# Performance work log

Measured on AMD Instinct MI355X. Metric: run time of the kernel, lower is better.

The kernel has to match this reference:

```python
import jax, jax.numpy as jnp
import numpy as np

N_QUBITS = 12
N_LAYERS = 4
BATCH = 4096
DIM = 2 ** N_QUBITS  # 4096


def _apply_1q(state, U, q):
    """Apply 2x2 complex gate U to qubit q. state: (B,) + (2,)*n, wire 0 = MSB (axis q+1)."""
    state = jnp.moveaxis(state, q + 1, -1)
    state = state @ U.T
    return jnp.moveaxis(state, -1, q + 1)


def _apply_cnot(state, c, t):
    """CNOT with control c, target t: flip target amplitudes where control bit == 1."""
    flipped = jnp.flip(state, axis=t + 1)
    shape = [2 if i == c + 1 else 1 for i in range(state.ndim)]
    ctrl = jnp.arange(2).reshape(shape)
    return jnp.where(ctrl == 1, flipped, state)


def setup_inputs() -> dict:
    key = jax.random.key(0)
    k1, k2 = jax.random.split(key)
    x = jax.random.normal(k1, (BATCH, DIM), dtype=jnp.float32)
    weights = jax.random.normal(k2, (N_LAYERS, N_QUBITS, 2), dtype=jnp.float32) * 0.1
    return {"x": x, "weights": weights}


def reference(x, weights):
    n, L = N_QUBITS, N_LAYERS
    B = x.shape[0]
    # AmplitudeEmbedding with normalize=True
    norm = jnp.linalg.norm(x, axis=-1, keepdims=True)
    state = (x / norm).astype(jnp.complex64).reshape((B,) + (2,) * n)
    for layer in range(L):
        for q in range(n):
            ty = weights[layer, q, 0]
            tz = weights[layer, q, 1]
            c, s = jnp.cos(ty / 2), jnp.sin(ty / 2)
            em = jnp.exp(-0.5j * tz.astype(jnp.complex64))  # e^{-i tz/2}
            ep = jnp.exp(+0.5j * tz.astype(jnp.complex64))
            # U = RZ(tz) @ RY(ty), fused single 2x2 gate per qubit
            U = jnp.stack([
                jnp.stack([c * em, -s * em]),
                jnp.stack([s * ep, c * ep]),
            ]).astype(jnp.complex64)
            state = _apply_1q(state, U, q)
        for q in range(n - 1):
            state = _apply_cnot(state, q, q + 1)
        if n > 2:
            state = _apply_cnot(state, n - 1, 0)
    probs = jnp.abs(state) ** 2  # (B,) + (2,)*n, float32
    reduce_axes = tuple(range(1, probs.ndim))
    outs = []
    for q in range(n):
        shape = [2 if i == q + 1 else 1 for i in range(probs.ndim)]
        sign = jnp.array([1.0, -1.0], dtype=probs.dtype).reshape(shape)
        outs.append(jnp.sum(probs * sign, axis=reduce_axes))
    return jnp.stack(outs, axis=-1)  # (B, n_qubits) <Z_q> expvals
```

## Files before the change

### kernel.cpp

```cpp
#include <hip/hip_runtime.h>

#define NQ   12
#define DIM  4096
#define NL   4
#define BLK  512

typedef unsigned short u16;
typedef unsigned int   u32;
typedef float f2 __attribute__((ext_vector_type(2)));

static constexpr int par(u32 v){ return __builtin_popcount(v)&1; }
static constexpr int hb(u16 v){ for(int i=11;i>=0;--i) if((v>>i)&1u) return i; return -1; }

struct L12 { u16 b[NQ]; };

static constexpr u32 lap(const L12& A, u32 x){ u32 r=0; for(int p=0;p<NQ;++p) if((x>>p)&1u) r^=A.b[p]; return r; }
static constexpr L12 lcomp(const L12& A, const L12& B){ L12 r{}; for(int p=0;p<NQ;++p) r.b[p]=(u16)lap(A,(u32)B.b[p]); return r; }
static constexpr L12 lident(){ L12 r{}; for(int p=0;p<NQ;++p) r.b[p]=(u16)(1u<<p); return r; }

static constexpr u32 applyT(u32 i){
  i ^= ((i>>0)&1u) << 11;
  for(int q=10;q>=0;--q){ int pc2=11-q, pt=10-q; i ^= ((i>>pc2)&1u) << pt; }
  return i;
}
static constexpr L12 lT(){ L12 t{}; for(int p=0;p<NQ;++p) t.b[p]=(u16)applyT(1u<<p); return t; }

static constexpr L12 linv(const L12& A){
  u16 v[NQ]={}; u16 u[NQ]={};
  for(int p=0;p<NQ;++p){ v[p]=A.b[p]; u[p]=(u16)(1u<<p); }
  for(int t=0;t<NQ;++t){
    int p=t; while(!((v[p]>>t)&1u)) ++p;
    u16 tv=v[p]; v[p]=v[t]; v[t]=tv; u16 tu=u[p]; u[p]=u[t]; u[t]=tu;
    for(int k=0;k<NQ;++k) if(k!=t && ((v[k]>>t)&1u)){ v[k]^=v[t]; u[k]^=u[t]; }
  }
  L12 r{}; for(int p=0;p<NQ;++p) r.b[p]=u[p]; return r;
}
static constexpr L12 ltr(const L12& A){
  L12 r{}; for(int p=0;p<NQ;++p) for(int q=0;q<NQ;++q) if((A.b[p]>>q)&1u) r.b[q]=(u16)(r.b[q]|(1u<<p));
  return r;
}

struct Tables {
  u16 cm[12][16];
  u16 wg[12][4];
  u16 wexp[NQ];
};

static constexpr Tables make_tables(){
  Tables tb{};
  const L12 T   = lT();
  const L12 Tit = ltr(linv(T));
  L12 A = lident();
  L12 W = lident();
  for(int l=0;l<NL;++l){
    for(int g=0;g<3;++g){
      const int st = l*3+g;
      u16 mm[4]={0,0,0,0};
      for(int i=0;i<4;++i){ mm[i]=A.b[4*g+i]; tb.wg[st][i]=W.b[4*g+i]; }
      for(int c=0;c<16;++c){ u32 m=0; for(int i=0;i<4;++i) if((c>>i)&1) m^=mm[i]; tb.cm[st][c]=(u16)m; }
    }
    A = lcomp(A, T);
    W = lcomp(W, Tit);
  }
  for(int p=0;p<NQ;++p) tb.wexp[p]=W.b[p];
  return tb;
}

static constexpr u16 UIMG[12] = {1,2,4,8, 3,5,6,7, 9,10,11,13};
static constexpr u32 swz(u32 j){
  u32 f=0;
  for(int k=4;k<12;++k) if((j>>k)&1u) f ^= (u32)UIMG[k];
  return j ^ (f & 15u);
}

struct Ech { u16 s[12]; };
static constexpr u16 ered(const Ech& e, u16 x){
  while(x){
    const int lb=hb(x);
    if(e.s[lb]) x=(u16)(x^e.s[lb]); else break;
  }
  return x;
}
static constexpr bool eadd(Ech& e, u16 x){
  x=ered(e,x); if(!x) return false;
  e.s[hb(x)]=x; return true;
}

struct Trip {
  u32 lane_c[9];
  u32 raw9[9];
  u32 smb[3];
  u32 rawm[3];
  u32 scmb[8];
  u32 cinv[3];
  u32 rho[3];
  bool cok;
};

static constexpr Trip make_trip(int t){
  Trip r{};
  const Tables tb = make_tables();
  u16 M[3]={}, w[3]={};
  for(int j=0;j<3;++j){
    const int g=3*t+j, st=g>>2, qi=g&3;
    M[j]=tb.cm[st][(u32)1<<qi]; w[j]=tb.wg[st][qi];
  }
  Ech em{};
  for(int j=0;j<3;++j) eadd(em,M[j]);
  bool isp[12]={};
  for(int b2=0;b2<12;++b2) if(em.s[b2]) isp[b2]=true;
  int np[12]={}; int nn=0;
  for(int p=0;p<12;++p) if(!isp[p]) np[nn++]=p;
  int s0=0,s1=1,s2=2,s3=3; bool found=false;
  for(int i0=0;i0<nn&&!found;++i0)for(int i1=i0+1;i1<nn&&!found;++i1)
  for(int i2=i1+1;i2<nn&&!found;++i2)for(int i3=i2+1;i3<nn&&!found;++i3){
    u16 img[4]={(u16)(swz((u32)1<<np[i0])&15u),(u16)(swz((u32)1<<np[i1])&15u),
                (u16)(swz((u32)1<<np[i2])&15u),(u16)(swz((u32)1<<np[i3])&15u)};
    u16 bas[4]={0,0,0,0}; int rk=0;
    for(int ii=0;ii<4;++ii){
      u16 x=img[ii];
      while(x){
        int hbx=3; while(hbx>0 && !((x>>hbx)&1)) --hbx;
        if(bas[hbx]) x=(u16)(x^bas[hbx]); else { bas[hbx]=x; ++rk; x=0; }
      }
    }
    if(rk==4){ s0=i0;s1=i1;s2=i2;s3=i3; found=true; }
  }
  int ord[9]={}; ord[0]=s0;ord[1]=s1;ord[2]=s2;ord[3]=s3;
  int rp=4;
  for(int j=0;j<nn;++j){ if(j!=s0&&j!=s1&&j!=s2&&j!=s3) ord[rp++]=j; }
  for(int k=0;k<9;++k){
    const int f=np[ord[k]];
    u32 nib=0;
    for(int i=0;i<3;++i) nib |= (u32)((w[i]>>f)&1u)<<i;
    r.lane_c[k]=(swz((u32)1<<f)<<3)|(nib<<28);
    r.raw9[k]=(u32)1<<f;
  }
  for(int k=0;k<3;++k){ r.smb[k]=swz((u32)M[k])<<3; r.rawm[k]=(u32)M[k]; }
  for(int c=0;c<8;++c){
    u32 m=0;
    for(int j=0;j<3;++j) if((c>>j)&1) m^=(u32)M[j];
    r.scmb[c]=swz(m)<<3;
  }
  u32 beta[3]={};
  for(int i=0;i<3;++i){ u32 row=0; for(int k=0;k<3;++k) row|=(u32)par((u32)(M[k]&w[i]))<<k; beta[i]=row; }
  u32 rows[3]={ beta[0]|(1u<<3), beta[1]|(2u<<3), beta[2]|(4u<<3) };
  bool ok=true;
  for(int col=0;col<3;++col){
    int pv=-1;
    for(int rr=col;rr<3;++rr) if((rows[rr]>>col)&1u){pv=rr;break;}
    if(pv<0){ok=false;break;}
    u32 tt=rows[col]; rows[col]=rows[pv]; rows[pv]=tt;
    for(int rr=0;rr<3;++rr) if(rr!=col&&((rows[rr]>>col)&1u)) rows[rr]^=rows[col];
  }
  r.cok=ok;
  if(ok) for(int k=0;k<3;++k) r.cinv[k]=(rows[k]>>3)&7u;
  for(int i=0;i<3;++i){
    u32 m=0;
    for(int c=0;c<8;++c){
      int v=0;
      for(int j=0;j<3;++j) if(j!=i && ((c>>j)&1)) v ^= (int)((beta[i]>>j)&1u);
      m |= (u32)v<<c;
    }
    r.rho[i]=m;
  }
  return r;
}

static constexpr Trip TRIPS[16] = {
  make_trip(0), make_trip(1), make_trip(2), make_trip(3),
  make_trip(4), make_trip(5), make_trip(6), make_trip(7),
  make_trip(8), make_trip(9), make_trip(10), make_trip(11),
  make_trip(12), make_trip(13), make_trip(14), make_trip(15)
};

struct RD { u16 pm[12]; u16 mu[12]; };
static constexpr RD make_rd(){
  RD r{};
  const Tables tb=make_tables();
  u16 M[3]={};
  for(int j=0;j<3;++j) M[j]=tb.cm[11][(u32)1<<(1+j)];
  for(int q=0;q<12;++q){
    r.pm[q]=tb.wexp[11-q];
    u32 m=0;
    for(int j=0;j<3;++j) m|=(u32)par((u32)(M[j]&tb.wexp[11-q]))<<j;
    r.mu[q]=(u16)m;
  }
  return r;
}
static constexpr RD RDT = make_rd();

__device__ __forceinline__ float fx(float a, u32 m){ return __uint_as_float(__float_as_uint(a)^m); }

template<int TI, int J>
__device__ __forceinline__ void one_gate(f2 (&a)[8], const float4* __restrict__ gw,
                                         const float4* __restrict__ gwH, u32 nib){
  constexpr int G = 3*TI+J;
  constexpr bool WITHW = (G < 36);
  const float4 g = gw[G];
  if constexpr (TRIPS[TI].cok){
#pragma unroll
    for(int c=0;c<8;++c){
      if((c>>J)&1) continue;
      const int c1=c|(1<<J);
      const int p = ((TRIPS[TI].rho[J]>>c)&1u) ? c1 : c;
      const int q = ((TRIPS[TI].rho[J]>>c)&1u) ? c : c1;
      f2 u,v;
      u.x=fmaf(-g.x,a[q].x,a[p].x); u.y=fmaf(-g.x,a[q].y,a[p].y);
      v.x=fmaf( g.y,u.x,a[q].x);    v.y=fmaf( g.y,u.y,a[q].y);
      a[p].x=fmaf(-g.x,v.x,u.x);    a[p].y=fmaf(-g.x,v.y,u.y);
      if(WITHW){ const float tt=fmaf(-g.z,v.y,v.x); v.y=fmaf(g.w,tt,v.y); v.x=fmaf(-g.z,v.y,tt); }
      a[q]=v;
    }
  } else {
    const u32 Rm = ((nib>>J)&1u)<<31;
    const float tg=fx(g.x,Rm), sg=fx(g.y,Rm);
    float t2=0.f, s2=0.f;
    if constexpr (WITHW){
      const float4 h=gwH[G];
      t2=fx(h.x,Rm^0x80000000u); s2=fx(h.y,Rm^0x80000000u);
    }
#pragma unroll
    for(int c=0;c<8;++c){
      if((c>>J)&1) continue;
      const int c1=c|(1<<J);
      if(((TRIPS[TI].rho[J]>>c)&1u)==0){
        f2 u,v;
        u.x=fmaf(-tg,a[c1].x,a[c].x); u.y=fmaf(-tg,a[c1].y,a[c].y);
        v.x=fmaf( sg,u.x,a[c1].x);    v.y=fmaf( sg,u.y,a[c1].y);
        a[c].x=fmaf(-tg,v.x,u.x);     a[c].y=fmaf(-tg,v.y,u.y);
        a[c1]=v;
        if(WITHW){
          float tt=fmaf(-t2,a[c].y,a[c].x);   a[c].y=fmaf( s2,tt,a[c].y);   a[c].x=fmaf(-t2,a[c].y,tt);
          tt=fmaf( t2,a[c1].y,a[c1].x);       a[c1].y=fmaf(-s2,tt,a[c1].y); a[c1].x=fmaf( t2,a[c1].y,tt);
        }
      } else {
        f2 u,v;
        u.x=fmaf( tg,a[c1].x,a[c].x); u.y=fmaf( tg,a[c1].y,a[c].y);
        v.x=fmaf(-sg,u.x,a[c1].x);    v.y=fmaf(-sg,u.y,a[c1].y);
        a[c].x=fmaf( tg,v.x,u.x);     a[c].y=fmaf( tg,v.y,u.y);
        a[c1]=v;
        if(WITHW){
          float tt=fmaf( t2,a[c].y,a[c].x);   a[c].y=fmaf(-s2,tt,a[c].y);   a[c].x=fmaf( t2,a[c].y,tt);
          tt=fmaf(-t2,a[c1].y,a[c1].x);       a[c1].y=fmaf( s2,tt,a[c1].y); a[c1].x=fmaf(-t2,a[c1].y,tt);
        }
      }
    }
  }
}

template<int TI>
__device__ __forceinline__ void trip_mid(const u32* msk, char* lds,
                                         const float4* __restrict__ gw,
                                         const float4* __restrict__ gwH){
  u32 acc=0;
#pragma unroll
  for(int k=0;k<9;++k) acc ^= TRIPS[TI].lane_c[k]&msk[k];
  const u32 nib = acc>>28;
  u32 base = acc & 0x0FFFFFFFu;
  if constexpr (TRIPS[TI].cok){
#pragma unroll
    for(int k=0;k<3;++k){
      const u32 sk=(u32)(__popc(TRIPS[TI].cinv[k]&nib)&1);
      base ^= TRIPS[TI].smb[k]&(0u-sk);
    }
  }
  f2 a[8]; u32 ad[8];
#pragma unroll
  for(int c=0;c<8;++c){ ad[c]=base^TRIPS[TI].scmb[c]; a[c]=*(const f2*)(lds+ad[c]); }
  one_gate<TI,0>(a,gw,gwH,nib);
  one_gate<TI,1>(a,gw,gwH,nib);
  one_gate<TI,2>(a,gw,gwH,nib);
#pragma unroll
  for(int c=0;c<8;++c){ *(f2*)(lds+ad[c])=a[c]; }
  __syncthreads();
}

__global__ void prep_kernel(const float* __restrict__ w, float4* __restrict__ gw,
                            float4* __restrict__ gwH){
  const int t = threadIdx.x;
  if(t < NL*NQ){
    const int l=t/NQ, p=t%NQ, q=(NQ-1)-p;
    const float ty=w[(l*NQ+q)*2+0], tz=w[(l*NQ+q)*2+1];
    gw[t]=make_float4(tanf(0.25f*ty), sinf(0.5f*ty), tanf(0.5f*tz), sinf(tz));
    gwH[t]=make_float4(tanf(0.25f*tz), sinf(0.5f*tz), 0.f, 0.f);
  }
}

__global__ __launch_bounds__(BLK, 8) void qsim_kernel(const float* __restrict__ x,
                                                      const float4* __restrict__ gw,
                                                      const float4* __restrict__ gwH,
                                                      float* __restrict__ out)
{
  __shared__ f2 st2[DIM];
  char* lds = (char*)st2;
  const int tid = threadIdx.x;
  const int bb  = blockIdx.x;

  u32 msk[9];
#pragma unroll
  for(int k=0;k<9;++k) msk[k]=0u-((u32)(tid>>k)&1u);

  {
    u32 acc=0, raw=0;
#pragma unroll
    for(int k=0;k<9;++k){ acc ^= TRIPS[0].lane_c[k]&msk[k]; raw ^= TRIPS[0].raw9[k]&msk[k]; }
    const u32 base = acc & 0x0FFFFFFFu;
    f2 a[8];
    const float* xr = x + (size_t)bb*DIM + raw;
    const float4 v0 = *reinterpret_cast<const float4*>(xr);
    const float4 v1 = *reinterpret_cast<const float4*>(xr+4);
    a[0]=(f2){v0.x,0.f}; a[1]=(f2){v0.y,0.f}; a[2]=(f2){v0.z,0.f}; a[3]=(f2){v0.w,0.f};
    a[4]=(f2){v1.x,0.f}; a[5]=(f2){v1.y,0.f}; a[6]=(f2){v1.z,0.f}; a[7]=(f2){v1.w,0.f};
    one_gate<0,0>(a,gw,gwH,0u);
    one_gate<0,1>(a,gw,gwH,0u);
    one_gate<0,2>(a,gw,gwH,0u);
#pragma unroll
    for(int c=0;c<8;++c){ *(f2*)(lds + (base^TRIPS[0].scmb[c])) = a[c]; }
    __syncthreads();
  }

  trip_mid<1 >(msk,lds,gw,gwH);
  trip_mid<2 >(msk,lds,gw,gwH);
  trip_mid<3 >(msk,lds,gw,gwH);
  trip_mid<4 >(msk,lds,gw,gwH);
  trip_mid<5 >(msk,lds,gw,gwH);
  trip_mid<6 >(msk,lds,gw,gwH);
  trip_mid<7 >(msk,lds,gw,gwH);
  trip_mid<8 >(msk,lds,gw,gwH);
  trip_mid<9 >(msk,lds,gw,gwH);
  trip_mid<10>(msk,lds,gw,gwH);
  trip_mid<11>(msk,lds,gw,gwH);
  trip_mid<12>(msk,lds,gw,gwH);
  trip_mid<13>(msk,lds,gw,gwH);
  trip_mid<14>(msk,lds,gw,gwH);

  {
    u32 acc=0, urep=0;
#pragma unroll
    for(int k=0;k<9;++k){ acc ^= TRIPS[15].lane_c[k]&msk[k]; urep ^= TRIPS[15].raw9[k]&msk[k]; }
    const u32 nib = acc>>28;
    u32 base = acc & 0x0FFFFFFFu;
    if constexpr (TRIPS[15].cok){
#pragma unroll
      for(int k=0;k<3;++k){
        const u32 sk=(u32)(__popc(TRIPS[15].cinv[k]&nib)&1);
        const u32 mi=0u-sk;
        base ^= TRIPS[15].smb[k]&mi; urep ^= TRIPS[15].rawm[k]&mi;
      }
    }
    f2 a[8];
#pragma unroll
    for(int c=0;c<8;++c){ a[c]=*(const f2*)(lds + (base^TRIPS[15].scmb[c])); }
    one_gate<15,0>(a,gw,gwH,nib);
    one_gate<15,1>(a,gw,gwH,nib);
    one_gate<15,2>(a,gw,gwH,nib);

    float pr[8];
#pragma unroll
    for(int c=0;c<8;++c) pr[c]=fmaf(a[c].x,a[c].x, a[c].y*a[c].y);
#pragma unroll
    for(int b=1;b<8;b<<=1){
#pragma unroll
      for(int c=0;c<8;++c){
        if(c&b) continue;
        const float u=pr[c], v=pr[c|b];
        pr[c]=u+v; pr[c|b]=u-v;
      }
    }
    float accq[12];
#pragma unroll
    for(int q=0;q<12;++q){
      const u32 sb = ((u32)__popc(urep & (u32)RDT.pm[q]) & 1u)<<31;
      accq[q]=__uint_as_float(__float_as_uint(pr[RDT.mu[q]])^sb);
    }
    float nrm2 = pr[0];
#pragma unroll
    for(int o=32;o;o>>=1){
      nrm2 += __shfl_xor(nrm2,o);
#pragma unroll
      for(int q=0;q<12;++q) accq[q]+=__shfl_xor(accq[q],o);
    }
    __syncthreads();
    float* wredf = (float*)lds;
    const int wid=tid>>6;
    if((tid&63)==0){
#pragma unroll
      for(int q=0;q<12;++q) wredf[wid*13+q]=accq[q];
      wredf[wid*13+12]=nrm2;
    }
    __syncthreads();
    if(tid<NQ){
      float s0=0.f, sn=0.f;
#pragma unroll
      for(int wv=0;wv<8;++wv){ s0+=wredf[wv*13+tid]; sn+=wredf[wv*13+12]; }
      out[(size_t)bb*NQ+tid]=s0/sn;
    }
  }
}

extern "C" void kernel_launch(void* const* d_in, const int* in_sizes, int n_in,
                              void* d_out, int out_size, void* d_ws, size_t ws_size,
                              hipStream_t stream) {
  const float* x = (const float*)d_in[0];
  const float* w = (const float*)d_in[1];
  float* out = (float*)d_out;
  float4* gw  = (float4*)d_ws;
  float4* gwH = gw + NL*NQ;
  const int B = in_sizes[0] / DIM;
  prep_kernel<<<1, 64, 0, stream>>>(w, gw, gwH);
  qsim_kernel<<<B, BLK, 0, stream>>>(x, gw, gwH, out);
}
```

Before: 121.9 us.

## Process six qubits per LDS pass with one wave holding 64 amplitudes per lane

Each LDS round trip now applies six fused gates instead of three. Each of the 64 threads holds 64 complex amplitudes in registers, and the block shrinks from 512 threads to a single wave. This cuts the number of LDS exchanges and barriers per sample from 16 to 8 and removes the cross-wave reduction. In exchange, register pressure becomes very high (128+ floats per lane), which risks spills. Only one wave per block also limits latency hiding, unless occupancy across blocks makes up for it.

```diff
diff --git a/kernel.cpp b/kernel.cpp
--- a/kernel.cpp
+++ b/kernel.cpp
@@ -3,14 +3,14 @@
 #define NQ   12
 #define DIM  4096
 #define NL   4
-#define BLK  512
+#define BLK  64
 
 typedef unsigned short u16;
 typedef unsigned int   u32;
+typedef unsigned long long u64;
 typedef float f2 __attribute__((ext_vector_type(2)));
 
 static constexpr int par(u32 v){ return __builtin_popcount(v)&1; }
-static constexpr int hb(u16 v){ for(int i=11;i>=0;--i) if((v>>i)&1u) return i; return -1; }
 
 struct L12 { u16 b[NQ]; };
 
@@ -41,9 +41,9 @@
 }
 
 struct Tables {
-  u16 cm[12][16];
-  u16 wg[12][4];
-  u16 wexp[NQ];
+  u16 A[NL][12];
+  u16 W[NL][12];
+  u16 wexp[12];
 };
 
 static constexpr Tables make_tables(){
@@ -53,16 +53,11 @@
   L12 A = lident();
   L12 W = lident();
   for(int l=0;l<NL;++l){
-    for(int g=0;g<3;++g){
-      const int st = l*3+g;
-      u16 mm[4]={0,0,0,0};
-      for(int i=0;i<4;++i){ mm[i]=A.b[4*g+i]; tb.wg[st][i]=W.b[4*g+i]; }
-      for(int c=0;c<16;++c){ u32 m=0; for(int i=0;i<4;++i) if((c>>i)&1) m^=mm[i]; tb.cm[st][c]=(u16)m; }
-    }
+    for(int p=0;p<12;++p){ tb.A[l][p]=A.b[p]; tb.W[l][p]=W.b[p]; }
     A = lcomp(A, T);
     W = lcomp(W, Tit);
   }
-  for(int p=0;p<NQ;++p) tb.wexp[p]=W.b[p];
+  for(int p=0;p<12;++p) tb.wexp[p]=W.b[p];
   return tb;
 }
 
@@ -73,143 +68,138 @@
   return j ^ (f & 15u);
 }
 
-struct Ech { u16 s[12]; };
-static constexpr u16 ered(const Ech& e, u16 x){
-  while(x){
-    const int lb=hb(x);
-    if(e.s[lb]) x=(u16)(x^e.s[lb]); else break;
-  }
-  return x;
-}
-static constexpr bool eadd(Ech& e, u16 x){
-  x=ered(e,x); if(!x) return false;
-  e.s[hb(x)]=x; return true;
-}
-
-struct Trip {
-  u32 lane_c[9];
-  u32 raw9[9];
-  u32 smb[3];
-  u32 rawm[3];
-  u32 scmb[8];
-  u32 cinv[3];
-  u32 rho[3];
+struct Trip6 {
+  u32 lane_c[6];
+  u32 raw6[6];
+  u32 smb[6];
+  u32 rawm[6];
+  u32 scmb[64];
+  u32 cinv[6];
+  u64 rho[6];
   bool cok;
 };
 
-static constexpr Trip make_trip(int t){
-  Trip r{};
+static constexpr Trip6 make_trip(int t){
+  Trip6 r{};
   const Tables tb = make_tables();
-  u16 M[3]={}, w[3]={};
-  for(int j=0;j<3;++j){
-    const int g=3*t+j, st=g>>2, qi=g&3;
-    M[j]=tb.cm[st][(u32)1<<qi]; w[j]=tb.wg[st][qi];
-  }
-  Ech em{};
-  for(int j=0;j<3;++j) eadd(em,M[j]);
-  bool isp[12]={};
-  for(int b2=0;b2<12;++b2) if(em.s[b2]) isp[b2]=true;
+  const int l = t>>1, h = (t&1)*6;
+  u16 M[6]={}, w[6]={};
+  for(int j=0;j<6;++j){ M[j]=tb.A[l][h+j]; w[j]=tb.W[l][h+j]; }
+  u16 ech[12]={};
+  for(int j=0;j<6;++j){
+    u16 x=M[j];
+    while(x){
+      int lb=11; while(!((x>>lb)&1)) --lb;
+      if(ech[lb]) x=(u16)(x^ech[lb]); else { ech[lb]=x; break; }
+    }
+  }
   int np[12]={}; int nn=0;
-  for(int p=0;p<12;++p) if(!isp[p]) np[nn++]=p;
-  int s0=0,s1=1,s2=2,s3=3; bool found=false;
-  for(int i0=0;i0<nn&&!found;++i0)for(int i1=i0+1;i1<nn&&!found;++i1)
-  for(int i2=i1+1;i2<nn&&!found;++i2)for(int i3=i2+1;i3<nn&&!found;++i3){
-    u16 img[4]={(u16)(swz((u32)1<<np[i0])&15u),(u16)(swz((u32)1<<np[i1])&15u),
-                (u16)(swz((u32)1<<np[i2])&15u),(u16)(swz((u32)1<<np[i3])&15u)};
-    u16 bas[4]={0,0,0,0}; int rk=0;
-    for(int ii=0;ii<4;++ii){
-      u16 x=img[ii];
-      while(x){
-        int hbx=3; while(hbx>0 && !((x>>hbx)&1)) --hbx;
-        if(bas[hbx]) x=(u16)(x^bas[hbx]); else { bas[hbx]=x; ++rk; x=0; }
+  for(int p=0;p<12;++p) if(!ech[p]) np[nn++]=p;
+  int ord[6]={0,1,2,3,4,5};
+  {
+    int bi=-1;
+    for(int ms=0; ms<64 && bi<0; ++ms){
+      if(__builtin_popcount((unsigned)ms)!=4) continue;
+      u16 bas[4]={0,0,0,0}; int rk=0;
+      for(int k=0;k<6;++k){
+        if(!((ms>>k)&1)) continue;
+        u16 x=(u16)(swz(1u<<np[k])&15u);
+        while(x){
+          int hb2=3; while(hb2>0&&!((x>>hb2)&1))--hb2;
+          if(bas[hb2]) x=(u16)(x^bas[hb2]); else { bas[hb2]=x; ++rk; x=0; }
+        }
       }
-    }
-    if(rk==4){ s0=i0;s1=i1;s2=i2;s3=i3; found=true; }
-  }
-  int ord[9]={}; ord[0]=s0;ord[1]=s1;ord[2]=s2;ord[3]=s3;
-  int rp=4;
-  for(int j=0;j<nn;++j){ if(j!=s0&&j!=s1&&j!=s2&&j!=s3) ord[rp++]=j; }
-  for(int k=0;k<9;++k){
-    const int f=np[ord[k]];
+      if(rk==4) bi=ms;
+    }
+    if(bi>=0){
+      int tmp[6]={}; int lo=0, hi=4;
+      for(int k=0;k<6;++k){ if((bi>>k)&1) tmp[lo++]=k; else tmp[hi++]=k; }
+      for(int k=0;k<6;++k) ord[k]=tmp[k];
+    }
+  }
+  for(int k=0;k<6;++k){
+    const int pos=np[ord[k]];
     u32 nib=0;
-    for(int i=0;i<3;++i) nib |= (u32)((w[i]>>f)&1u)<<i;
-    r.lane_c[k]=(swz((u32)1<<f)<<3)|(nib<<28);
-    r.raw9[k]=(u32)1<<f;
-  }
-  for(int k=0;k<3;++k){ r.smb[k]=swz((u32)M[k])<<3; r.rawm[k]=(u32)M[k]; }
-  for(int c=0;c<8;++c){
+    for(int i=0;i<6;++i) nib |= (u32)((w[i]>>pos)&1u)<<i;
+    r.lane_c[k] = (swz(1u<<pos)<<3)|(nib<<26);
+    r.raw6[k]=1u<<pos;
+  }
+  for(int i=0;i<6;++i){ r.smb[i]=swz((u32)M[i])<<3; r.rawm[i]=(u32)M[i]; }
+  for(int c=0;c<64;++c){
     u32 m=0;
-    for(int j=0;j<3;++j) if((c>>j)&1) m^=(u32)M[j];
+    for(int j=0;j<6;++j) if((c>>j)&1) m^=(u32)M[j];
     r.scmb[c]=swz(m)<<3;
   }
-  u32 beta[3]={};
-  for(int i=0;i<3;++i){ u32 row=0; for(int k=0;k<3;++k) row|=(u32)par((u32)(M[k]&w[i]))<<k; beta[i]=row; }
-  u32 rows[3]={ beta[0]|(1u<<3), beta[1]|(2u<<3), beta[2]|(4u<<3) };
+  u32 Cm[6]={};
+  for(int i=0;i<6;++i){ u32 row=0; for(int k=0;k<6;++k) row|=(u32)par((u32)(M[k]&w[i]))<<k; Cm[i]=row; }
+  u32 rows[6]={};
+  for(int i=0;i<6;++i) rows[i]=Cm[i]|(1u<<(6+i));
   bool ok=true;
-  for(int col=0;col<3;++col){
+  for(int col=0;col<6;++col){
     int pv=-1;
-    for(int rr=col;rr<3;++rr) if((rows[rr]>>col)&1u){pv=rr;break;}
+    for(int rr=col;rr<6;++rr) if((rows[rr]>>col)&1u){pv=rr;break;}
     if(pv<0){ok=false;break;}
     u32 tt=rows[col]; rows[col]=rows[pv]; rows[pv]=tt;
-    for(int rr=0;rr<3;++rr) if(rr!=col&&((rows[rr]>>col)&1u)) rows[rr]^=rows[col];
+    for(int rr=0;rr<6;++rr) if(rr!=col && ((rows[rr]>>col)&1u)) rows[rr]^=rows[col];
   }
   r.cok=ok;
-  if(ok) for(int k=0;k<3;++k) r.cinv[k]=(rows[k]>>3)&7u;
-  for(int i=0;i<3;++i){
-    u32 m=0;
-    for(int c=0;c<8;++c){
+  if(ok) for(int k=0;k<6;++k) r.cinv[k]=(rows[k]>>6)&63u;
+  for(int i=0;i<6;++i){
+    u64 m=0;
+    for(int c=0;c<64;++c){
       int v=0;
-      for(int j=0;j<3;++j) if(j!=i && ((c>>j)&1)) v ^= (int)((beta[i]>>j)&1u);
-      m |= (u32)v<<c;
+      for(int k=0;k<6;++k) if(k!=i && ((c>>k)&1)) v ^= (int)((Cm[i]>>k)&1u);
+      m |= (u64)v<<c;
     }
     r.rho[i]=m;
   }
   return r;
 }
 
-static constexpr Trip TRIPS[16] = {
-  make_trip(0), make_trip(1), make_trip(2), make_trip(3),
-  make_trip(4), make_trip(5), make_trip(6), make_trip(7),
-  make_trip(8), make_trip(9), make_trip(10), make_trip(11),
-  make_trip(12), make_trip(13), make_trip(14), make_trip(15)
-};
+static constexpr Trip6 TR0 = make_trip(0);
+static constexpr Trip6 TR1 = make_trip(1);
+static constexpr Trip6 TR2 = make_trip(2);
+static constexpr Trip6 TR3 = make_trip(3);
+static constexpr Trip6 TR4 = make_trip(4);
+static constexpr Trip6 TR5 = make_trip(5);
+static constexpr Trip6 TR6 = make_trip(6);
+static constexpr Trip6 TR7 = make_trip(7);
+__device__ constexpr Trip6 TRIPS[8] = {TR0,TR1,TR2,TR3,TR4,TR5,TR6,TR7};
 
 struct RD { u16 pm[12]; u16 mu[12]; };
 static constexpr RD make_rd(){
   RD r{};
   const Tables tb=make_tables();
-  u16 M[3]={};
-  for(int j=0;j<3;++j) M[j]=tb.cm[11][(u32)1<<(1+j)];
   for(int q=0;q<12;++q){
     r.pm[q]=tb.wexp[11-q];
     u32 m=0;
-    for(int j=0;j<3;++j) m|=(u32)par((u32)(M[j]&tb.wexp[11-q]))<<j;
+    for(int j=0;j<6;++j) m|=(u32)par((u32)(tb.A[3][6+j]&tb.wexp[11-q]))<<j;
     r.mu[q]=(u16)m;
   }
   return r;
 }
-static constexpr RD RDT = make_rd();
+__device__ constexpr RD RDT = make_rd();
 
 __device__ __forceinline__ float fx(float a, u32 m){ return __uint_as_float(__float_as_uint(a)^m); }
 
 template<int TI, int J>
-__device__ __forceinline__ void one_gate(f2 (&a)[8], const float4* __restrict__ gw,
+__device__ __forceinline__ void one_gate(f2 (&a)[64], const float4* __restrict__ gw,
                                          const float4* __restrict__ gwH, u32 nib){
-  constexpr int G = 3*TI+J;
-  constexpr bool WITHW = (G < 36);
+  constexpr int G = TI*6+J;
+  constexpr bool WITHW = (TI < 6);
   const float4 g = gw[G];
   if constexpr (TRIPS[TI].cok){
 #pragma unroll
-    for(int c=0;c<8;++c){
+    for(int c=0;c<64;++c){
       if((c>>J)&1) continue;
       const int c1=c|(1<<J);
-      const int p = ((TRIPS[TI].rho[J]>>c)&1u) ? c1 : c;
-      const int q = ((TRIPS[TI].rho[J]>>c)&1u) ? c : c1;
+      const bool sw = (TRIPS[TI].rho[J]>>c)&1ull;
+      const int p = sw?c1:c, q = sw?c:c1;
       f2 u,v;
       u.x=fmaf(-g.x,a[q].x,a[p].x); u.y=fmaf(-g.x,a[q].y,a[p].y);
       v.x=fmaf( g.y,u.x,a[q].x);    v.y=fmaf( g.y,u.y,a[q].y);
       a[p].x=fmaf(-g.x,v.x,u.x);    a[p].y=fmaf(-g.x,v.y,u.y);
-      if(WITHW){ const float tt=fmaf(-g.z,v.y,v.x); v.y=fmaf(g.w,tt,v.y); v.x=fmaf(-g.z,v.y,tt); }
+      if(WITHW){ const float t=fmaf(-g.z,v.y,v.x); v.y=fmaf(g.w,t,v.y); v.x=fmaf(-g.z,v.y,t); }
       a[q]=v;
     }
   } else {
@@ -217,14 +207,14 @@
     const float tg=fx(g.x,Rm), sg=fx(g.y,Rm);
     float t2=0.f, s2=0.f;
     if constexpr (WITHW){
-      const float4 h=gwH[G];
-      t2=fx(h.x,Rm^0x80000000u); s2=fx(h.y,Rm^0x80000000u);
-    }
-#pragma unroll
-    for(int c=0;c<8;++c){
+      const float4 hh=gwH[G];
+      t2=fx(hh.x,Rm^0x80000000u); s2=fx(hh.y,Rm^0x80000000u);
+    }
+#pragma unroll
+    for(int c=0;c<64;++c){
       if((c>>J)&1) continue;
       const int c1=c|(1<<J);
-      if(((TRIPS[TI].rho[J]>>c)&1u)==0){
+      if(((TRIPS[TI].rho[J]>>c)&1ull)==0){
         f2 u,v;
         u.x=fmaf(-tg,a[c1].x,a[c].x); u.y=fmaf(-tg,a[c1].y,a[c].y);
         v.x=fmaf( sg,u.x,a[c1].x);    v.y=fmaf( sg,u.y,a[c1].y);
@@ -250,29 +240,32 @@
 }
 
 template<int TI>
-__device__ __forceinline__ void trip_mid(const u32* msk, char* lds,
+__device__ __forceinline__ void mid_trip(const u32* msk, char* lds,
                                          const float4* __restrict__ gw,
                                          const float4* __restrict__ gwH){
   u32 acc=0;
 #pragma unroll
-  for(int k=0;k<9;++k) acc ^= TRIPS[TI].lane_c[k]&msk[k];
-  const u32 nib = acc>>28;
-  u32 base = acc & 0x0FFFFFFFu;
+  for(int k=0;k<6;++k) acc ^= TRIPS[TI].lane_c[k]&msk[k];
+  const u32 nib = acc>>26;
+  u32 base = acc & 0x03FFFFFFu;
   if constexpr (TRIPS[TI].cok){
 #pragma unroll
-    for(int k=0;k<3;++k){
-      const u32 sk=(u32)(__popc(TRIPS[TI].cinv[k]&nib)&1);
-      base ^= TRIPS[TI].smb[k]&(0u-sk);
-    }
-  }
-  f2 a[8]; u32 ad[8];
-#pragma unroll
-  for(int c=0;c<8;++c){ ad[c]=base^TRIPS[TI].scmb[c]; a[c]=*(const f2*)(lds+ad[c]); }
+    for(int k=0;k<6;++k){
+      const u32 ak=(u32)(__popc(TRIPS[TI].cinv[k]&nib)&1);
+      base ^= TRIPS[TI].smb[k]&(0u-ak);
+    }
+  }
+  f2 a[64];
+#pragma unroll
+  for(int c=0;c<64;++c) a[c]=*(const f2*)(lds+(base^TRIPS[TI].scmb[c]));
   one_gate<TI,0>(a,gw,gwH,nib);
   one_gate<TI,1>(a,gw,gwH,nib);
   one_gate<TI,2>(a,gw,gwH,nib);
-#pragma unroll
-  for(int c=0;c<8;++c){ *(f2*)(lds+ad[c])=a[c]; }
+  one_gate<TI,3>(a,gw,gwH,nib);
+  one_gate<TI,4>(a,gw,gwH,nib);
+  one_gate<TI,5>(a,gw,gwH,nib);
+#pragma unroll
+  for(int c=0;c<64;++c) *(f2*)(lds+(base^TRIPS[TI].scmb[c]))=a[c];
   __syncthreads();
 }
 
@@ -287,82 +280,82 @@
   }
 }
 
-__global__ __launch_bounds__(BLK, 8) void qsim_kernel(const float* __restrict__ x,
-                                                      const float4* __restrict__ gw,
-                                                      const float4* __restrict__ gwH,
-                                                      float* __restrict__ out)
+__global__ __launch_bounds__(BLK) void qsim_kernel(const float* __restrict__ x,
+                                                   const float4* __restrict__ gw,
+                                                   const float4* __restrict__ gwH,
+                                                   float* __restrict__ out)
 {
   __shared__ f2 st2[DIM];
   char* lds = (char*)st2;
   const int tid = threadIdx.x;
   const int bb  = blockIdx.x;
 
-  u32 msk[9];
-#pragma unroll
-  for(int k=0;k<9;++k) msk[k]=0u-((u32)(tid>>k)&1u);
+  u32 msk[6];
+#pragma unroll
+  for(int k=0;k<6;++k) msk[k]=0u-((u32)(tid>>k)&1u);
 
   {
     u32 acc=0, raw=0;
 #pragma unroll
-    for(int k=0;k<9;++k){ acc ^= TRIPS[0].lane_c[k]&msk[k]; raw ^= TRIPS[0].raw9[k]&msk[k]; }
-    const u32 base = acc & 0x0FFFFFFFu;
-    f2 a[8];
+    for(int k=0;k<6;++k){ acc ^= TRIPS[0].lane_c[k]&msk[k]; raw ^= TRIPS[0].raw6[k]&msk[k]; }
+    const u32 base = acc & 0x03FFFFFFu;
+    f2 a[64];
     const float* xr = x + (size_t)bb*DIM + raw;
-    const float4 v0 = *reinterpret_cast<const float4*>(xr);
-    const float4 v1 = *reinterpret_cast<const float4*>(xr+4);
-    a[0]=(f2){v0.x,0.f}; a[1]=(f2){v0.y,0.f}; a[2]=(f2){v0.z,0.f}; a[3]=(f2){v0.w,0.f};
-    a[4]=(f2){v1.x,0.f}; a[5]=(f2){v1.y,0.f}; a[6]=(f2){v1.z,0.f}; a[7]=(f2){v1.w,0.f};
+#pragma unroll
+    for(int s=0;s<16;++s){
+      const float4 v = *reinterpret_cast<const float4*>(xr + 4*s);
+      a[4*s+0]=(f2){v.x,0.f}; a[4*s+1]=(f2){v.y,0.f};
+      a[4*s+2]=(f2){v.z,0.f}; a[4*s+3]=(f2){v.w,0.f};
+    }
     one_gate<0,0>(a,gw,gwH,0u);
     one_gate<0,1>(a,gw,gwH,0u);
     one_gate<0,2>(a,gw,gwH,0u);
-#pragma unroll
-    for(int c=0;c<8;++c){ *(f2*)(lds + (base^TRIPS[0].scmb[c])) = a[c]; }
+    one_gate<0,3>(a,gw,gwH,0u);
+    one_gate<0,4>(a,gw,gwH,0u);
+    one_gate<0,5>(a,gw,gwH,0u);
+#pragma unroll
+    for(int c=0;c<64;++c) *(f2*)(lds+(base^TRIPS[0].scmb[c]))=a[c];
     __syncthreads();
   }
 
-  trip_mid<1 >(msk,lds,gw,gwH);
-  trip_mid<2 >(msk,lds,gw,gwH);
-  trip_mid<3 >(msk,lds,gw,gwH);
-  trip_mid<4 >(msk,lds,gw,gwH);
-  trip_mid<5 >(msk,lds,gw,gwH);
-  trip_mid<6 >(msk,lds,gw,gwH);
-  trip_mid<7 >(msk,lds,gw,gwH);
-  trip_mid<8 >(msk,lds,gw,gwH);
-  trip_mid<9 >(msk,lds,gw,gwH);
-  trip_mid<10>(msk,lds,gw,gwH);
-  trip_mid<11>(msk,lds,gw,gwH);
-  trip_mid<12>(msk,lds,gw,gwH);
-  trip_mid<13>(msk,lds,gw,gwH);
-  trip_mid<14>(msk,lds,gw,gwH);
+  mid_trip<1>(msk,lds,gw,gwH);
+  mid_trip<2>(msk,lds,gw,gwH);
+  mid_trip<3>(msk,lds,gw,gwH);
+  mid_trip<4>(msk,lds,gw,gwH);
+  mid_trip<5>(msk,lds,gw,gwH);
+  mid_trip<6>(msk,lds,gw,gwH);
 
   {
     u32 acc=0, urep=0;
 #pragma unroll
-    for(int k=0;k<9;++k){ acc ^= TRIPS[15].lane_c[k]&msk[k]; urep ^= TRIPS[15].raw9[k]&msk[k]; }
-    const u32 nib = acc>>28;
-    u32 base = acc & 0x0FFFFFFFu;
-    if constexpr (TRIPS[15].cok){
-#pragma unroll
-      for(int k=0;k<3;++k){
-        const u32 sk=(u32)(__popc(TRIPS[15].cinv[k]&nib)&1);
-        const u32 mi=0u-sk;
-        base ^= TRIPS[15].smb[k]&mi; urep ^= TRIPS[15].rawm[k]&mi;
+    for(int k=0;k<6;++k){ acc ^= TRIPS[7].lane_c[k]&msk[k]; urep ^= TRIPS[7].raw6[k]&msk[k]; }
+    const u32 nib = acc>>26;
+    u32 base = acc & 0x03FFFFFFu;
+    if constexpr (TRIPS[7].cok){
+#pragma unroll
+      for(int k=0;k<6;++k){
+        const u32 ak=(u32)(__popc(TRIPS[7].cinv[k]&nib)&1);
+        const u32 mi=0u-ak;
+        base ^= TRIPS[7].smb[k]&mi; urep ^= TRIPS[7].rawm[k]&mi;
       }
     }
-    f2 a[8];
-#pragma unroll
-    for(int c=0;c<8;++c){ a[c]=*(const f2*)(lds + (base^TRIPS[15].scmb[c])); }
-    one_gate<15,0>(a,gw,gwH,nib);
-    one_gate<15,1>(a,gw,gwH,nib);
-    one_gate<15,2>(a,gw,gwH,nib);
-
-    float pr[8];
-#pragma unroll
-    for(int c=0;c<8;++c) pr[c]=fmaf(a[c].x,a[c].x, a[c].y*a[c].y);
-#pragma unroll
-    for(int b=1;b<8;b<<=1){
-#pragma unroll
-      for(int c=0;c<8;++c){
+    f2 a[64];
+#pragma unroll
+    for(int c=0;c<64;++c) a[c]=*(const f2*)(lds+(base^TRIPS[7].scmb[c]));
+    one_gate<7,0>(a,gw,gwH,nib);
+    one_gate<7,1>(a,gw,gwH,nib);
+    one_gate<7,2>(a,gw,gwH,nib);
+    one_gate<7,3>(a,gw,gwH,nib);
+    one_gate<7,4>(a,gw,gwH,nib);
+    one_gate<7,5>(a,gw,gwH,nib);
+
+    float pr[64];
+#pragma unroll
+    for(int c=0;c<64;++c) pr[c]=fmaf(a[c].x,a[c].x, a[c].y*a[c].y);
+#pragma unroll
+    for(int b=1;b<64;b<<=1){
+#pragma unroll
+      for(int c=0;c<64;++c){
         if(c&b) continue;
         const float u=pr[c], v=pr[c|b];
         pr[c]=u+v; pr[c|b]=u-v;
@@ -374,27 +367,17 @@
       const u32 sb = ((u32)__popc(urep & (u32)RDT.pm[q]) & 1u)<<31;
       accq[q]=__uint_as_float(__float_as_uint(pr[RDT.mu[q]])^sb);
     }
-    float nrm2 = pr[0];
+    float nrm = pr[0];
 #pragma unroll
     for(int o=32;o;o>>=1){
-      nrm2 += __shfl_xor(nrm2,o);
+      nrm += __shfl_xor(nrm,o);
 #pragma unroll
       for(int q=0;q<12;++q) accq[q]+=__shfl_xor(accq[q],o);
     }
-    __syncthreads();
-    float* wredf = (float*)lds;
-    const int wid=tid>>6;
-    if((tid&63)==0){
-#pragma unroll
-      for(int q=0;q<12;++q) wredf[wid*13+q]=accq[q];
-      wredf[wid*13+12]=nrm2;
-    }
-    __syncthreads();
-    if(tid<NQ){
-      float s0=0.f, sn=0.f;
-#pragma unroll
-      for(int wv=0;wv<8;++wv){ s0+=wredf[wv*13+tid]; sn+=wredf[wv*13+12]; }
-      out[(size_t)bb*NQ+tid]=s0/sn;
+    if(tid==0){
+      const float rn = 1.0f/nrm;
+#pragma unroll
+      for(int q=0;q<12;++q) out[(size_t)bb*NQ+q]=accq[q]*rn;
     }
   }
 }
```

Result: slower. 130.5 us (+7.0%).
